# Optimization experiments

Hardware: AMD Instinct MI355X
Metric: run time of the kernel (lower is better)

## Reference

```python
import jax, jax.numpy as jnp
import numpy as np

N_SEL = 8192
N_FEAT = 256
K_SUB = 256
N_PERS = 4
E_FULL = 262144
E_RAW = 262144
N_TOTAL = 8192
EPSILON = 0.5
LAMB1 = 0.5


def setup_inputs() -> dict:
    key = jax.random.key(0)
    ks = jax.random.split(key, 8)
    x = jax.random.normal(ks[0], (N_SEL, N_FEAT), dtype=jnp.float32)
    metric_weight = jax.random.uniform(ks[1], (N_PERS, N_FEAT), dtype=jnp.float32)
    selected_batch = jnp.sort(jax.random.randint(ks[2], (N_SEL,), 0, K_SUB, dtype=jnp.int32))
    selected_mapping = jax.random.randint(ks[3], (N_SEL,), 0, N_TOTAL, dtype=jnp.int32)
    selected_belong = jax.random.randint(ks[4], (K_SUB,), 0, K_SUB, dtype=jnp.int32)
    selected_score = jax.random.uniform(ks[5], (K_SUB,), dtype=jnp.float32)
    full_edge_index = jax.random.randint(ks[6], (2, E_FULL), 0, N_SEL, dtype=jnp.int32)
    raw_edge_index = jax.random.randint(ks[7], (2, E_RAW), 0, N_TOTAL, dtype=jnp.int32)
    return {"x": x, "metric_weight": metric_weight, "selected_batch": selected_batch,
            "selected_mapping": selected_mapping, "selected_belong": selected_belong,
            "selected_score": selected_score, "full_edge_index": full_edge_index,
            "raw_edge_index": raw_edge_index, "n_total": N_TOTAL}


def weighted_cosine(x, w):
    # x: [N, D], w: [P, D] -> mean over P perspectives of cosine sim
    h = x[None, :, :] * w[:, None, :]                        # [P, N, D]
    h = h / (jnp.linalg.norm(h, axis=-1, keepdims=True) + 1e-12)
    return jnp.einsum('pnd,pmd->nm', h, h) / w.shape[0]      # [N, N]


def reference(x, metric_weight, selected_batch, selected_mapping, selected_belong,
              selected_score, full_edge_index, raw_edge_index, n_total):
    n_sel = x.shape[0]
    k_sub = selected_score.shape[0]
    # scatter score normalization: scores of subgraphs sharing a 'belong' group sum to 1
    score_sum = jax.ops.segment_sum(selected_score, selected_belong, num_segments=k_sub)
    score = selected_score / score_sum[selected_belong]
    # z_node = x (no encoder); weighted-cosine metric over all selected nodes
    adj = weighted_cosine(x, metric_weight)                  # [N_sel, N_sel]
    # mask to allowed intra-subgraph edges (full_edge_index)
    mask = jnp.zeros_like(adj).at[full_edge_index[0], full_edge_index[1]].set(1.0)
    adj = adj * mask
    # postprocess: EpsilonNN threshold, then remove self loops
    adj = adj * (adj > EPSILON).astype(adj.dtype)
    diag = jnp.arange(n_sel)
    adj = adj.at[diag, diag].set(0.0)
    # per-edge weight = normalized score of the source node's subgraph, times lamb1
    adj_w = adj * (score[selected_batch] * LAMB1)[:, None]
    # map selected-node indices to global node ids and coalesce (sum duplicates)
    tmp = jnp.zeros((n_total, n_sel), adj.dtype).at[selected_mapping].add(adj_w)
    out = jnp.zeros((n_total, n_total), adj.dtype).at[:, selected_mapping].add(tmp)
    # add raw graph with weight (1 - lamb1); coalesce == dense scatter-add
    out = out.at[raw_edge_index[0], raw_edge_index[1]].add(1.0 - LAMB1)
    return out
```

## Files before the change

kernel.cpp:

```cpp
#include <hip/hip_runtime.h>

typedef float f4 __attribute__((ext_vector_type(4)));

#define N_SEL   8192
#define N_FEAT  256
#define K_SUB   256
#define N_PERS  4
#define E_FULL  262144
#define E_RAW   262144
#define N_TOTAL 8192
#define EPSILON 0.5f
#define LAMB1   0.5f

#define WS_SCORE_OFF  (128 * 1024)
#define WS_CNT_OFF    (132 * 1024)
#define WS_XQ_OFF     (256 * 1024)
#define WS_LIST_OFF   (WS_XQ_OFF + 2 * 1024 * 1024)

__global__ __launch_bounds__(256) void prep_kernel(const f4* __restrict__ x4,
                                                   const f4* __restrict__ w4,
                                                   float* __restrict__ invn,
                                                   unsigned int* __restrict__ xq,
                                                   const float* __restrict__ s,
                                                   const int* __restrict__ belong,
                                                   float* __restrict__ score,
                                                   int* __restrict__ cnt) {
    __shared__ float sv[K_SUB];
    __shared__ int bv[K_SUB];
    int gid = blockIdx.x * 256 + threadIdx.x;
    int wave = gid >> 6;
    int lane = threadIdx.x & 63;
    int n = wave >> 2;
    int p = wave & 3;
    f4 xv = x4[(size_t)n * 64 + lane];
    f4 wv = w4[p * 64 + lane];
    if (p == 0) {
        int pk = 0;
        pk = __builtin_amdgcn_cvt_pk_fp8_f32(xv.x, xv.y, pk, false);
        pk = __builtin_amdgcn_cvt_pk_fp8_f32(xv.z, xv.w, pk, true);
        xq[(size_t)n * 64 + lane] = (unsigned int)pk;
    }
    f4 h = xv * wv;
    float ss = h.x * h.x + h.y * h.y + h.z * h.z + h.w * h.w;
    #pragma unroll
    for (int off = 32; off; off >>= 1) ss += __shfl_xor(ss, off);
    if (lane == 0) invn[n * 4 + p] = 1.0f / (sqrtf(ss) + 1e-12f);

    if (gid == 0) *cnt = 0;

    if (blockIdx.x == 0) {
        int t = threadIdx.x;
        sv[t] = s[t];
        bv[t] = belong[t];
        __syncthreads();
        int myb = bv[t];
        float sum = 0.0f;
        for (int k = 0; k < K_SUB; ++k)
            if (bv[k] == myb) sum += sv[k];
        score[t] = sv[t] / sum;
    }
}

__global__ __launch_bounds__(256) void zero_edge_kernel(f4* __restrict__ out4,
                                                        const unsigned int* __restrict__ xq,
                                                        const f4* __restrict__ w4,
                                                        const int* __restrict__ fe,
                                                        const int* __restrict__ sel_batch,
                                                        const f4* __restrict__ invn4,
                                                        const float* __restrict__ score,
                                                        int2* __restrict__ list,
                                                        int* __restrict__ cnt) {
    int b = blockIdx.x;
    int t = threadIdx.x;
    int lane = t & 63;
    int w = t >> 6;

    int ebase = b * 128 + w * 32;
    int myidx = (lane < 32) ? fe[ebase + lane] : fe[E_FULL + ebase + (lane - 32)];

    f4 q0 = w4[0 * 64 + lane]; q0 *= q0;
    f4 q1 = w4[1 * 64 + lane]; q1 *= q1;
    f4 q2 = w4[2 * 64 + lane]; q2 *= q2;
    f4 q3 = w4[3 * 64 + lane]; q3 *= q3;

    size_t obase = (size_t)(b * 4 + w) * 2048;
    f4 z = (f4)0.0f;

    int ci = __shfl(myidx, 0);
    int cj = __shfl(myidx, 32);
    unsigned int xi = xq[(size_t)ci * 64 + lane];
    unsigned int xj = xq[(size_t)cj * 64 + lane];
    f4 ii = invn4[ci];
    f4 ij = invn4[cj];

    #pragma unroll 4
    for (int s = 0; s < 32; ++s) {
        out4[obase + s * 64 + lane] = z;

        int i = ci, j = cj;
        unsigned int ax = xi, bx = xj;
        f4 aii = ii, aij = ij;
        if (s < 31) {
            ci = __shfl(myidx, s + 1);
            cj = __shfl(myidx, 32 + s + 1);
            xi = xq[(size_t)ci * 64 + lane];
            xj = xq[(size_t)cj * 64 + lane];
            ii = invn4[ci];
            ij = invn4[cj];
        }

        float pd0 = __builtin_amdgcn_cvt_f32_fp8((int)ax, 0) *
                    __builtin_amdgcn_cvt_f32_fp8((int)bx, 0);
        float pd1 = __builtin_amdgcn_cvt_f32_fp8((int)ax, 1) *
                    __builtin_amdgcn_cvt_f32_fp8((int)bx, 1);
        float pd2 = __builtin_amdgcn_cvt_f32_fp8((int)ax, 2) *
                    __builtin_amdgcn_cvt_f32_fp8((int)bx, 2);
        float pd3 = __builtin_amdgcn_cvt_f32_fp8((int)ax, 3) *
                    __builtin_amdgcn_cvt_f32_fp8((int)bx, 3);

        float a0 = fmaf(pd3, q0.w, fmaf(pd2, q0.z, fmaf(pd1, q0.y, pd0 * q0.x)));
        float a1 = fmaf(pd3, q1.w, fmaf(pd2, q1.z, fmaf(pd1, q1.y, pd0 * q1.x)));
        float a2 = fmaf(pd3, q2.w, fmaf(pd2, q2.z, fmaf(pd1, q2.y, pd0 * q2.x)));
        float a3 = fmaf(pd3, q3.w, fmaf(pd2, q3.z, fmaf(pd1, q3.y, pd0 * q3.x)));

        float v = a0 * (aii.x * aij.x) + a1 * (aii.y * aij.y) +
                  a2 * (aii.z * aij.z) + a3 * (aii.w * aij.w);
        v += __shfl_xor(v, 1);
        v += __shfl_xor(v, 2);
        v += __shfl_xor(v, 4);
        v += __shfl_xor(v, 8);
        v += __shfl_xor(v, 16);
        v += __shfl_xor(v, 32);

        if (lane == 0 && i != j) {
            v *= 0.25f;
            if (v > EPSILON) {
                float val = v * score[sel_batch[i]] * LAMB1;
                int idx = atomicAdd(cnt, 1);
                int2 ent;
                ent.x = (i << 13) | j;
                ent.y = __float_as_int(val);
                list[idx] = ent;
            }
        }
    }
}

__global__ __launch_bounds__(256) void raw_finalize_kernel(const int* __restrict__ re,
                                                           const int2* __restrict__ list,
                                                           const int* __restrict__ cnt,
                                                           const int* __restrict__ sel_map,
                                                           float* __restrict__ out) {
    int t = blockIdx.x * 256 + threadIdx.x;
    if (t < E_RAW) {
        int u = re[t];
        int v = re[E_RAW + t];
        atomicAdd(&out[(size_t)u * N_TOTAL + v], 1.0f - LAMB1);
    }
    int n = *cnt;
    if (t < n) {
        int2 ek = list[t];
        bool first = true;
        for (int l = 0; l < t; ++l)
            if (list[l].x == ek.x) { first = false; break; }
        if (first) {
            int i = ek.x >> 13;
            int j = ek.x & (N_SEL - 1);
            atomicAdd(&out[(size_t)sel_map[i] * N_TOTAL + sel_map[j]],
                      __int_as_float(ek.y));
        }
    }
}

extern "C" void kernel_launch(void* const* d_in, const int* in_sizes, int n_in,
                              void* d_out, int out_size, void* d_ws, size_t ws_size,
                              hipStream_t stream) {
    const float* x         = (const float*)d_in[0];
    const float* mw        = (const float*)d_in[1];
    const int* sel_batch   = (const int*)d_in[2];
    const int* sel_map     = (const int*)d_in[3];
    const int* sel_belong  = (const int*)d_in[4];
    const float* sel_score = (const float*)d_in[5];
    const int* fe          = (const int*)d_in[6];
    const int* re          = (const int*)d_in[7];
    float* out             = (float*)d_out;

    char* ws         = (char*)d_ws;
    float* invn      = (float*)ws;
    float* score     = (float*)(ws + WS_SCORE_OFF);
    int* cnt         = (int*)(ws + WS_CNT_OFF);
    unsigned int* xq = (unsigned int*)(ws + WS_XQ_OFF);
    int2* list       = (int2*)(ws + WS_LIST_OFF);

    prep_kernel<<<8192, 256, 0, stream>>>(
        (const f4*)x, (const f4*)mw, invn, xq, sel_score, sel_belong, score, cnt);
    zero_edge_kernel<<<2048, 256, 0, stream>>>(
        (f4*)out, xq, (const f4*)mw, fe, sel_batch,
        (const f4*)invn, score, list, cnt);
    raw_finalize_kernel<<<1024, 256, 0, stream>>>(re, list, cnt, sel_map, out);
}
```

Before: 88.98 us.

## Bin raw edges into per-row cells and fold them into the output zero-fill

A new scatter kernel buckets raw edges into 256-column cells (up to four packed column bytes per cell), and anything beyond four goes to an overflow list. The zero-fill pass then writes 0.5 values for those edges directly, so most scattered global atomics on the 256 MB output disappear. Only overflow edges and selected edges are handled atomically in finalize. prep_kernel also computes all four perspective norms per wave, using a quarter of the blocks, and clears the cell arrays. The cost is an extra launch and extra workspace traffic for the cell arrays.

Measured after the change: 109.2 us. +22.7%, slower.

```diff
diff --git a/kernel.cpp b/kernel.cpp
--- a/kernel.cpp
+++ b/kernel.cpp
@@ -12,41 +12,60 @@
 #define EPSILON 0.5f
 #define LAMB1   0.5f
 
-#define WS_SCORE_OFF  (128 * 1024)
-#define WS_CNT_OFF    (132 * 1024)
-#define WS_XQ_OFF     (256 * 1024)
-#define WS_LIST_OFF   (WS_XQ_OFF + 2 * 1024 * 1024)
+#define WS_SCORE_OFF (128 * 1024)
+#define WS_CNT_OFF   (132 * 1024)
+#define WS_CF_OFF    (256 * 1024)
+#define WS_CELLS_OFF (WS_CF_OFF + 1024 * 1024)
+#define WS_XQ_OFF    (WS_CELLS_OFF + 1024 * 1024)
+#define WS_LIST_OFF  (WS_XQ_OFF + 2 * 1024 * 1024)
+#define WS_OVF_OFF   (WS_LIST_OFF + 2 * 1024 * 1024)
 
 __global__ __launch_bounds__(256) void prep_kernel(const f4* __restrict__ x4,
                                                    const f4* __restrict__ w4,
-                                                   float* __restrict__ invn,
+                                                   f4* __restrict__ invn4,
                                                    unsigned int* __restrict__ xq,
                                                    const float* __restrict__ s,
                                                    const int* __restrict__ belong,
                                                    float* __restrict__ score,
-                                                   int* __restrict__ cnt) {
+                                                   int* __restrict__ cnts,
+                                                   unsigned int* __restrict__ cellfill,
+                                                   unsigned int* __restrict__ cells) {
     __shared__ float sv[K_SUB];
     __shared__ int bv[K_SUB];
     int gid = blockIdx.x * 256 + threadIdx.x;
-    int wave = gid >> 6;
+    int n = gid >> 6;
     int lane = threadIdx.x & 63;
-    int n = wave >> 2;
-    int p = wave & 3;
+
     f4 xv = x4[(size_t)n * 64 + lane];
-    f4 wv = w4[p * 64 + lane];
-    if (p == 0) {
-        int pk = 0;
-        pk = __builtin_amdgcn_cvt_pk_fp8_f32(xv.x, xv.y, pk, false);
-        pk = __builtin_amdgcn_cvt_pk_fp8_f32(xv.z, xv.w, pk, true);
-        xq[(size_t)n * 64 + lane] = (unsigned int)pk;
-    }
-    f4 h = xv * wv;
-    float ss = h.x * h.x + h.y * h.y + h.z * h.z + h.w * h.w;
+
+    int pk = 0;
+    pk = __builtin_amdgcn_cvt_pk_fp8_f32(xv.x, xv.y, pk, false);
+    pk = __builtin_amdgcn_cvt_pk_fp8_f32(xv.z, xv.w, pk, true);
+    xq[(size_t)n * 64 + lane] = (unsigned int)pk;
+
+    f4 ssv;
     #pragma unroll
-    for (int off = 32; off; off >>= 1) ss += __shfl_xor(ss, off);
-    if (lane == 0) invn[n * 4 + p] = 1.0f / (sqrtf(ss) + 1e-12f);
-
-    if (gid == 0) *cnt = 0;
+    for (int p = 0; p < 4; ++p) {
+        f4 h = xv * w4[p * 64 + lane];
+        float ss = h.x * h.x + h.y * h.y + h.z * h.z + h.w * h.w;
+        #pragma unroll
+        for (int off = 32; off; off >>= 1) ss += __shfl_xor(ss, off);
+        ssv[p] = ss;
+    }
+    if (lane == 0) {
+        f4 r;
+        r.x = 1.0f / (sqrtf(ssv.x) + 1e-12f);
+        r.y = 1.0f / (sqrtf(ssv.y) + 1e-12f);
+        r.z = 1.0f / (sqrtf(ssv.z) + 1e-12f);
+        r.w = 1.0f / (sqrtf(ssv.w) + 1e-12f);
+        invn4[n] = r;
+    }
+
+    if (gid < N_TOTAL * 32) {
+        cellfill[gid] = 0;
+        cells[gid] = 0;
+    }
+    if (gid < 2) cnts[gid] = 0;
 
     if (blockIdx.x == 0) {
         int t = threadIdx.x;
@@ -61,6 +80,26 @@
     }
 }
 
+__global__ __launch_bounds__(256) void scatter_kernel(const int* __restrict__ re,
+                                                      unsigned int* __restrict__ cellfill,
+                                                      unsigned int* __restrict__ cells,
+                                                      int2* __restrict__ ovf,
+                                                      int* __restrict__ cnts) {
+    int t = blockIdx.x * 256 + threadIdx.x;
+    if (t >= E_RAW) return;
+    int u = re[t];
+    int v = re[E_RAW + t];
+    int cell = u * 32 + (v >> 8);
+    unsigned pos = atomicAdd(&cellfill[cell], 1u);
+    if (pos < 4) {
+        atomicOr(&cells[cell], ((unsigned)(v & 255)) << (8 * pos));
+    } else {
+        int oi = atomicAdd(&cnts[1], 1);
+        int2 e; e.x = u; e.y = v;
+        ovf[oi] = e;
+    }
+}
+
 __global__ __launch_bounds__(256) void zero_edge_kernel(f4* __restrict__ out4,
                                                         const unsigned int* __restrict__ xq,
                                                         const f4* __restrict__ w4,
@@ -68,8 +107,10 @@
                                                         const int* __restrict__ sel_batch,
                                                         const f4* __restrict__ invn4,
                                                         const float* __restrict__ score,
+                                                        const unsigned int* __restrict__ cellfill,
+                                                        const unsigned int* __restrict__ cells,
                                                         int2* __restrict__ list,
-                                                        int* __restrict__ cnt) {
+                                                        int* __restrict__ cnts) {
     int b = blockIdx.x;
     int t = threadIdx.x;
     int lane = t & 63;
@@ -83,8 +124,14 @@
     f4 q2 = w4[2 * 64 + lane]; q2 *= q2;
     f4 q3 = w4[3 * 64 + lane]; q3 *= q3;
 
-    size_t obase = (size_t)(b * 4 + w) * 2048;
-    f4 z = (f4)0.0f;
+    int rowid = b * 4 + w;
+    size_t obase = (size_t)rowid * 2048;
+
+    unsigned ccnt = 0, cpack = 0;
+    if (lane < 32) {
+        ccnt  = cellfill[rowid * 32 + lane];
+        cpack = cells[rowid * 32 + lane];
+    }
 
     int ci = __shfl(myidx, 0);
     int cj = __shfl(myidx, 32);
@@ -95,7 +142,19 @@
 
     #pragma unroll 4
     for (int s = 0; s < 32; ++s) {
-        out4[obase + s * 64 + lane] = z;
+        unsigned cs = __shfl(ccnt, s);
+        unsigned cp = __shfl(cpack, s);
+        f4 zz = (f4)0.0f;
+        if (cs) {
+            #pragma unroll
+            for (int e = 0; e < 4; ++e) {
+                if ((unsigned)e < cs) {
+                    unsigned c8 = (cp >> (8 * e)) & 255u;
+                    if ((int)(c8 >> 2) == lane) zz[c8 & 3] += (1.0f - LAMB1);
+                }
+            }
+        }
+        out4[obase + s * 64 + lane] = zz;
 
         int i = ci, j = cj;
         unsigned int ax = xi, bx = xj;
@@ -136,7 +195,7 @@
             v *= 0.25f;
             if (v > EPSILON) {
                 float val = v * score[sel_batch[i]] * LAMB1;
-                int idx = atomicAdd(cnt, 1);
+                int idx = atomicAdd(&cnts[0], 1);
                 int2 ent;
                 ent.x = (i << 13) | j;
                 ent.y = __float_as_int(val);
@@ -146,18 +205,18 @@
     }
 }
 
-__global__ __launch_bounds__(256) void raw_finalize_kernel(const int* __restrict__ re,
-                                                           const int2* __restrict__ list,
-                                                           const int* __restrict__ cnt,
-                                                           const int* __restrict__ sel_map,
-                                                           float* __restrict__ out) {
+__global__ __launch_bounds__(256) void finalize_kernel(const int2* __restrict__ list,
+                                                       const int2* __restrict__ ovf,
+                                                       const int* __restrict__ cnts,
+                                                       const int* __restrict__ sel_map,
+                                                       float* __restrict__ out) {
     int t = blockIdx.x * 256 + threadIdx.x;
-    if (t < E_RAW) {
-        int u = re[t];
-        int v = re[E_RAW + t];
-        atomicAdd(&out[(size_t)u * N_TOTAL + v], 1.0f - LAMB1);
-    }
-    int n = *cnt;
+    int m = cnts[1];
+    if (t < m) {
+        int2 e = ovf[t];
+        atomicAdd(&out[(size_t)e.x * N_TOTAL + e.y], 1.0f - LAMB1);
+    }
+    int n = cnts[0];
     if (t < n) {
         int2 ek = list[t];
         bool first = true;
@@ -185,17 +244,22 @@
     const int* re          = (const int*)d_in[7];
     float* out             = (float*)d_out;
 
-    char* ws         = (char*)d_ws;
-    float* invn      = (float*)ws;
-    float* score     = (float*)(ws + WS_SCORE_OFF);
-    int* cnt         = (int*)(ws + WS_CNT_OFF);
-    unsigned int* xq = (unsigned int*)(ws + WS_XQ_OFF);
-    int2* list       = (int2*)(ws + WS_LIST_OFF);
-
-    prep_kernel<<<8192, 256, 0, stream>>>(
-        (const f4*)x, (const f4*)mw, invn, xq, sel_score, sel_belong, score, cnt);
+    char* ws           = (char*)d_ws;
+    f4* invn4          = (f4*)ws;
+    float* score       = (float*)(ws + WS_SCORE_OFF);
+    int* cnts          = (int*)(ws + WS_CNT_OFF);
+    unsigned int* cf   = (unsigned int*)(ws + WS_CF_OFF);
+    unsigned int* cel  = (unsigned int*)(ws + WS_CELLS_OFF);
+    unsigned int* xq   = (unsigned int*)(ws + WS_XQ_OFF);
+    int2* list         = (int2*)(ws + WS_LIST_OFF);
+    int2* ovf          = (int2*)(ws + WS_OVF_OFF);
+
+    prep_kernel<<<2048, 256, 0, stream>>>(
+        (const f4*)x, (const f4*)mw, invn4, xq, sel_score, sel_belong, score,
+        cnts, cf, cel);
+    scatter_kernel<<<E_RAW / 256, 256, 0, stream>>>(re, cf, cel, ovf, cnts);
     zero_edge_kernel<<<2048, 256, 0, stream>>>(
         (f4*)out, xq, (const f4*)mw, fe, sel_batch,
-        (const f4*)invn, score, list, cnt);
-    raw_finalize_kernel<<<1024, 256, 0, stream>>>(re, list, cnt, sel_map, out);
-}
+        invn4, score, cf, cel, list, cnts);
+    finalize_kernel<<<1024, 256, 0, stream>>>(list, ovf, cnts, sel_map, out);
+}
```
